# Kernel optimization log

Measured on AMD Instinct MI355X. Metric: run time of the kernel, lower is better.

## Reference

```python
import jax, jax.numpy as jnp
import numpy as np

N_NODES = 20000
N_EDGES = 320000
D_IN = 512
D_OUT = 512


def setup_inputs() -> dict:
    key = jax.random.key(0)
    k1, k2, k3, k4, k5, k6 = jax.random.split(key, 6)
    stdv = 1.0 / np.sqrt(D_OUT)
    return {
        "h": jax.random.normal(k1, (N_NODES, D_IN), dtype=jnp.float32),
        "weight": jax.random.uniform(k2, (D_IN, D_OUT), dtype=jnp.float32, minval=-stdv, maxval=stdv),
        "bias": jax.random.uniform(k3, (D_OUT,), dtype=jnp.float32, minval=-stdv, maxval=stdv),
        # GCN symmetric normalization term per node (deg^{-1/2}); strictly positive
        "norm": jax.random.uniform(k4, (N_NODES, 1), dtype=jnp.float32, minval=0.05, maxval=1.0),
        "src": jax.random.randint(k5, (N_EDGES,), 0, N_NODES, dtype=jnp.int32),
        "dst": jax.random.randint(k6, (N_EDGES,), 0, N_NODES, dtype=jnp.int32),
    }


def reference(h, weight, bias, norm, src, dst):
    # dropout p=0 -> identity (eval mode)
    # pre-normalize after dense projection: [N, d_out]
    hw = norm * jnp.matmul(h, weight)
    # update_all(copy_u, sum): gather source features, scatter-sum into dst
    msg = hw[src]  # [E, d_out]
    agg = jax.ops.segment_sum(msg, dst, num_segments=N_NODES)  # [N, d_out]
    out = agg * norm + bias
    return jax.nn.relu(out)
```

## Files before the change

### kernel.cpp

```cpp
#include <hip/hip_runtime.h>

#define M_NODES 20000
#define N_EDGES_C 320000
#define DIM 512

typedef __attribute__((ext_vector_type(4))) float f32x4;
typedef __attribute__((ext_vector_type(2))) float f32x2;
typedef __attribute__((ext_vector_type(4))) __bf16 bf16x4;
typedef __attribute__((ext_vector_type(8))) __bf16 bf16x8;

__device__ __forceinline__ void async16(__bf16* lds, const __bf16* g) {
  __builtin_amdgcn_global_load_lds(
      (const __attribute__((address_space(1))) void*)g,
      (__attribute__((address_space(3))) void*)lds, 16, 0, 0);
}

__global__ __launch_bounds__(256) void zero_k(int4* __restrict__ counts4) {
  const int i = blockIdx.x * 256 + threadIdx.x;
  if (i < M_NODES / 4) counts4[i] = int4{0, 0, 0, 0};
}

__global__ __launch_bounds__(256) void pre_k(const float* __restrict__ h,
                                             const float* __restrict__ w,
                                             const float* __restrict__ norm,
                                             const int* __restrict__ dst,
                                             __bf16* __restrict__ hb,
                                             __bf16* __restrict__ wT,
                                             int* __restrict__ counts) {
  const int bid = blockIdx.x;
  const int tid = threadIdx.x;
  const int gtid = bid * 256 + tid;
  const int gsz = gridDim.x * 256;

  const int nunits = (M_NODES / 32) * 8;
  for (int u = bid; u < nunits; u += gridDim.x) {
    const int p = u & 7;
    const int row = (u >> 3) * 32 + (tid >> 3);
    const int col = p * 64 + (tid & 7) * 8;
    const float s = norm[row];
    const float* hp = &h[(size_t)row * DIM + col];
    f32x4 v0 = *(const f32x4*)hp;
    f32x4 v1 = *(const f32x4*)(hp + 4);
    bf16x8 o;
    o[0] = (__bf16)(v0.x * s); o[1] = (__bf16)(v0.y * s);
    o[2] = (__bf16)(v0.z * s); o[3] = (__bf16)(v0.w * s);
    o[4] = (__bf16)(v1.x * s); o[5] = (__bf16)(v1.y * s);
    o[6] = (__bf16)(v1.z * s); o[7] = (__bf16)(v1.w * s);
    *(bf16x8*)&hb[(size_t)row * DIM + col] = o;
  }

  if (bid < 256) {
    __shared__ float tile[32][33];
    const int bx = (bid & 15) * 32, by = (bid >> 4) * 32;
    const int tx = tid & 31, ty8 = tid >> 5;
#pragma unroll
    for (int st = 0; st < 4; ++st) {
      const int r = ty8 + st * 8;
      tile[r][tx] = w[(by + r) * DIM + bx + tx];
    }
    __syncthreads();
#pragma unroll
    for (int st = 0; st < 4; ++st) {
      const int r = ty8 + st * 8;
      wT[(bx + r) * DIM + by + tx] = (__bf16)tile[tx][r];
    }
  }

  for (int e = gtid; e < N_EDGES_C; e += gsz) atomicAdd(&counts[dst[e]], 1);
}

__global__ __launch_bounds__(256) void scan_k(int* __restrict__ counts,
                                              int* __restrict__ offsets) {
  __shared__ int wsum2[4];
  const int tid = threadIdx.x;
  const int lane = tid & 63, wid = tid >> 6;
  const int base = tid * 80;
  int s = 0;
  if (tid < 250) {
#pragma unroll
    for (int i = 0; i < 80; i += 4) {
      int4 c = *(const int4*)&counts[base + i];
      s += c.x + c.y + c.z + c.w;
    }
  }
  int x = s;
#pragma unroll
  for (int off = 1; off < 64; off <<= 1) {
    int t = __shfl_up(x, off, 64);
    if (lane >= off) x += t;
  }
  if (lane == 63) wsum2[wid] = x;
  __syncthreads();
  int wbase = 0;
  for (int wI = 0; wI < wid; ++wI) wbase += wsum2[wI];
  int run = wbase + x - s;
  if (tid < 250) {
#pragma unroll
    for (int i = 0; i < 80; i += 4) {
      int4 c = *(const int4*)&counts[base + i];
      int4 o;
      o.x = run;
      o.y = run + c.x;
      o.z = o.y + c.y;
      o.w = o.z + c.z;
      *(int4*)&offsets[base + i] = o;
      *(int4*)&counts[base + i] = o;
      run = o.w + c.w;
    }
  }
  if (tid == 0) {
    int tot = 0;
#pragma unroll
    for (int wI = 0; wI < 4; ++wI) tot += wsum2[wI];
    offsets[M_NODES] = tot;
  }
}

__global__ __launch_bounds__(256) void fill_k(const int* __restrict__ src,
                                              const int* __restrict__ dst,
                                              int* __restrict__ cursor,
                                              int* __restrict__ esrc) {
  int e = blockIdx.x * 256 + threadIdx.x;
  if (e < N_EDGES_C) {
    int p = atomicAdd(&cursor[dst[e]], 1);
    esrc[p] = src[e];
  }
}

__global__ __launch_bounds__(256) void aggregate_k(const __bf16* __restrict__ hb,
                                                   const int* __restrict__ offs,
                                                   const int* __restrict__ esrc,
                                                   __bf16* __restrict__ aggb) {
  const int panel = blockIdx.x & 7;
  const int nb = blockIdx.x >> 3;
  const int wv = threadIdx.x >> 6;
  const int lane = threadIdx.x & 63;
  const int slot = lane >> 3;
  const int cg = lane & 7;
  const int node = nb * 32 + wv * 8 + slot;

  const int beg = offs[node], end = offs[node + 1];
  const size_t pbase = (size_t)panel * 64 + cg * 8;

  f32x2 a2[4] = {};
  int j = beg;
  while (j + 8 <= end) {
    const int idx = esrc[j + cg];
    int sid[8];
#pragma unroll
    for (int g = 0; g < 8; ++g) sid[g] = __shfl(idx, (lane & 56) + g, 64);
#pragma unroll
    for (int g = 0; g < 8; ++g) {
      const uint4 u = *(const uint4*)&hb[(size_t)sid[g] * DIM + pbase];
      f32x2 p0 = {__uint_as_float(u.x << 16), __uint_as_float(u.x & 0xFFFF0000u)};
      f32x2 p1 = {__uint_as_float(u.y << 16), __uint_as_float(u.y & 0xFFFF0000u)};
      f32x2 p2 = {__uint_as_float(u.z << 16), __uint_as_float(u.z & 0xFFFF0000u)};
      f32x2 p3 = {__uint_as_float(u.w << 16), __uint_as_float(u.w & 0xFFFF0000u)};
      a2[0] += p0; a2[1] += p1; a2[2] += p2; a2[3] += p3;
    }
    j += 8;
  }
  for (; j < end; ++j) {
    const uint4 u = *(const uint4*)&hb[(size_t)esrc[j] * DIM + pbase];
    f32x2 p0 = {__uint_as_float(u.x << 16), __uint_as_float(u.x & 0xFFFF0000u)};
    f32x2 p1 = {__uint_as_float(u.y << 16), __uint_as_float(u.y & 0xFFFF0000u)};
    f32x2 p2 = {__uint_as_float(u.z << 16), __uint_as_float(u.z & 0xFFFF0000u)};
    f32x2 p3 = {__uint_as_float(u.w << 16), __uint_as_float(u.w & 0xFFFF0000u)};
    a2[0] += p0; a2[1] += p1; a2[2] += p2; a2[3] += p3;
  }
  bf16x8 o;
#pragma unroll
  for (int q = 0; q < 4; ++q) {
    o[2 * q]     = (__bf16)a2[q].x;
    o[2 * q + 1] = (__bf16)a2[q].y;
  }
  *(bf16x8*)&aggb[(size_t)node * DIM + pbase] = o;
}

__global__ __launch_bounds__(256, 2) void gemm_k(const __bf16* __restrict__ A,
                                                 const __bf16* __restrict__ B,
                                                 const float* __restrict__ bias,
                                                 const float* __restrict__ norm,
                                                 float* __restrict__ C) {
  __shared__ __bf16 As[3][64 * 64];
  __shared__ __bf16 Bs[3][128 * 64];
  const int tid = threadIdx.x;
  const int lane = tid & 63;
  const int wv = tid >> 6;
  const int wr = wv >> 1, wc = wv & 1;
  const int m0 = blockIdx.x * 64;
  const int n0 = blockIdx.y * 128;

  f32x4 acc[2][4] = {};

  const int srow = tid >> 3;
  const int scol = ((tid & 7) ^ (srow & 7)) * 8;
  const int ldst = (tid & 7) * 8;

  auto stage = [&](int buf, int kt) {
    const int kb = kt * 64 + scol;
#pragma unroll
    for (int jj = 0; jj < 2; ++jj) {
      const int lrow = jj * 32 + srow;
      int arow = m0 + lrow;
      arow = arow < M_NODES ? arow : (M_NODES - 1);
      async16(&As[buf][lrow * 64 + ldst], A + (size_t)arow * DIM + kb);
    }
#pragma unroll
    for (int jj = 0; jj < 4; ++jj) {
      const int lrow = jj * 32 + srow;
      async16(&Bs[buf][lrow * 64 + ldst], B + (size_t)(n0 + lrow) * DIM + kb);
    }
  };

  stage(0, 0);
  stage(1, 1);

  int cb = 0;
  for (int kt = 0; kt < DIM / 64; ++kt) {
    if (kt < DIM / 64 - 1)
      asm volatile("s_waitcnt vmcnt(6)" ::: "memory");
    else
      asm volatile("s_waitcnt vmcnt(0)" ::: "memory");
    __builtin_amdgcn_s_barrier();
    asm volatile("" ::: "memory");

    if (kt + 2 < DIM / 64) {
      int sb = cb + 2; if (sb >= 3) sb -= 3;
      stage(sb, kt + 2);
    }

#pragma unroll
    for (int kk = 0; kk < 64; kk += 32) {
      const int c = (kk >> 3) + (lane >> 4);
      bf16x8 af[2], bfr[4];
#pragma unroll
      for (int m = 0; m < 2; ++m) {
        const int r = wr * 32 + m * 16 + (lane & 15);
        af[m] = *(const bf16x8*)&As[cb][r * 64 + ((c ^ (r & 7)) * 8)];
      }
#pragma unroll
      for (int n = 0; n < 4; ++n) {
        const int r = wc * 64 + n * 16 + (lane & 15);
        bfr[n] = *(const bf16x8*)&Bs[cb][r * 64 + ((c ^ (r & 7)) * 8)];
      }
#pragma unroll
      for (int m = 0; m < 2; ++m)
#pragma unroll
        for (int n = 0; n < 4; ++n)
          acc[m][n] = __builtin_amdgcn_mfma_f32_16x16x32_bf16(af[m], bfr[n], acc[m][n], 0, 0, 0);
    }
    cb = (cb == 2) ? 0 : cb + 1;
  }

#pragma unroll
  for (int m = 0; m < 2; ++m) {
    const int rbase = m0 + wr * 32 + m * 16 + (lane >> 4) * 4;
#pragma unroll
    for (int r = 0; r < 4; ++r) {
      const int row = rbase + r;
      if (row < M_NODES) {
        const float nv = norm[row];
#pragma unroll
        for (int n = 0; n < 4; ++n) {
          const int col = n0 + wc * 64 + n * 16 + (lane & 15);
          float v = acc[m][n][r] * nv + bias[col];
          C[(size_t)row * DIM + col] = v > 0.f ? v : 0.f;
        }
      }
    }
  }
}

#define HB_OFF   0UL
#define AGG_OFF  20480000UL
#define WT_OFF   40960000UL
#define CNT_OFF  41484288UL
#define OFS_OFF  41564288UL
#define ESRC_OFF 41644544UL
#define WS_NEEDED 42924544UL

extern "C" void kernel_launch(void* const* d_in, const int* in_sizes, int n_in,
                              void* d_out, int out_size, void* d_ws, size_t ws_size,
                              hipStream_t stream) {
  const float* h    = (const float*)d_in[0];
  const float* w    = (const float*)d_in[1];
  const float* bias = (const float*)d_in[2];
  const float* norm = (const float*)d_in[3];
  const int*   src  = (const int*)d_in[4];
  const int*   dst  = (const int*)d_in[5];
  float* out = (float*)d_out;

  if (ws_size < WS_NEEDED) return;

  char* ws = (char*)d_ws;
  __bf16* hb      = (__bf16*)(ws + HB_OFF);
  __bf16* aggb    = (__bf16*)(ws + AGG_OFF);
  __bf16* wT      = (__bf16*)(ws + WT_OFF);
  int*    counts  = (int*)(ws + CNT_OFF);
  int*    offsets = (int*)(ws + OFS_OFF);
  int*    esrc    = (int*)(ws + ESRC_OFF);

  zero_k<<<20, 256, 0, stream>>>((int4*)counts);
  pre_k<<<2048, 256, 0, stream>>>(h, w, norm, dst, hb, wT, counts);
  scan_k<<<1, 256, 0, stream>>>(counts, offsets);
  fill_k<<<1250, 256, 0, stream>>>(src, dst, counts, esrc);
  aggregate_k<<<5000, 256, 0, stream>>>(hb, offsets, esrc, aggb);
  gemm_k<<<dim3(313, 4), 256, 0, stream>>>(aggb, wT, bias, norm, out);
}
```

Baseline: 120.2 us.

## Restructure final GEMM: full-K A tile in LDS, B streamed from global into registers

The final GEMM becomes 625 blocks, each covering 32 rows and all 512 output columns. Each block loads a whole 32x512 A strip into swizzled LDS once, and each wave streams its 128-column slice of B straight from global memory (L2) into registers, double-buffered across k steps. This removes the triple-buffered LDS pipeline for B, the repeated A loading across four column blocks, and the per-k-tile barriers. In exchange, B fragments are re-read from L2 by every block, register pressure rises (16 accumulators plus 16 B fragments), and the row bounds check is dropped because 20000 divides evenly by 32.

Measured after the change: 144.2 us. +20.0%, slower.

```diff
diff --git a/kernel.cpp b/kernel.cpp
--- a/kernel.cpp
+++ b/kernel.cpp
@@ -177,96 +177,90 @@
   *(bf16x8*)&aggb[(size_t)node * DIM + pbase] = o;
 }
 
-__global__ __launch_bounds__(256, 2) void gemm_k(const __bf16* __restrict__ A,
-                                                 const __bf16* __restrict__ B,
-                                                 const float* __restrict__ bias,
-                                                 const float* __restrict__ norm,
-                                                 float* __restrict__ C) {
-  __shared__ __bf16 As[3][64 * 64];
-  __shared__ __bf16 Bs[3][128 * 64];
+__global__ __launch_bounds__(256) void gemm_k(const __bf16* __restrict__ A,
+                                              const __bf16* __restrict__ B,
+                                              const float* __restrict__ bias,
+                                              const float* __restrict__ norm,
+                                              float* __restrict__ C) {
+  __shared__ __bf16 As[32 * 512];
   const int tid = threadIdx.x;
   const int lane = tid & 63;
   const int wv = tid >> 6;
-  const int wr = wv >> 1, wc = wv & 1;
-  const int m0 = blockIdx.x * 64;
-  const int n0 = blockIdx.y * 128;
-
-  f32x4 acc[2][4] = {};
-
-  const int srow = tid >> 3;
-  const int scol = ((tid & 7) ^ (srow & 7)) * 8;
-  const int ldst = (tid & 7) * 8;
-
-  auto stage = [&](int buf, int kt) {
-    const int kb = kt * 64 + scol;
-#pragma unroll
-    for (int jj = 0; jj < 2; ++jj) {
-      const int lrow = jj * 32 + srow;
-      int arow = m0 + lrow;
-      arow = arow < M_NODES ? arow : (M_NODES - 1);
-      async16(&As[buf][lrow * 64 + ldst], A + (size_t)arow * DIM + kb);
-    }
-#pragma unroll
-    for (int jj = 0; jj < 4; ++jj) {
-      const int lrow = jj * 32 + srow;
-      async16(&Bs[buf][lrow * 64 + ldst], B + (size_t)(n0 + lrow) * DIM + kb);
-    }
-  };
-
-  stage(0, 0);
-  stage(1, 1);
-
-  int cb = 0;
-  for (int kt = 0; kt < DIM / 64; ++kt) {
-    if (kt < DIM / 64 - 1)
-      asm volatile("s_waitcnt vmcnt(6)" ::: "memory");
-    else
-      asm volatile("s_waitcnt vmcnt(0)" ::: "memory");
-    __builtin_amdgcn_s_barrier();
-    asm volatile("" ::: "memory");
-
-    if (kt + 2 < DIM / 64) {
-      int sb = cb + 2; if (sb >= 3) sb -= 3;
-      stage(sb, kt + 2);
-    }
-
-#pragma unroll
-    for (int kk = 0; kk < 64; kk += 32) {
-      const int c = (kk >> 3) + (lane >> 4);
-      bf16x8 af[2], bfr[4];
+  const int m0 = blockIdx.x * 32;
+
+#pragma unroll
+  for (int p = 0; p < 8; ++p) {
+    const int u = p * 256 + tid;
+    const int r = u >> 6;
+    const int c = u & 63;
+    const int g = c ^ (r & 7);
+    async16(&As[r * 512 + c * 8], A + (size_t)(m0 + r) * DIM + g * 8);
+  }
+  __syncthreads();
+
+  f32x4 acc[2][8] = {};
+  const int lr = lane & 15;
+  const int lc = lane >> 4;
+  const __bf16* __restrict__ bbase =
+      B + (size_t)(wv * 128 + lr) * DIM + lc * 8;
+
+  bf16x8 bA[8], bB[8];
+#pragma unroll
+  for (int n = 0; n < 8; ++n)
+    bA[n] = *(const bf16x8*)(bbase + (size_t)n * 16 * DIM);
+
+#pragma unroll
+  for (int kt = 0; kt < 16; kt += 2) {
+#pragma unroll
+    for (int n = 0; n < 8; ++n)
+      bB[n] = *(const bf16x8*)(bbase + (size_t)n * 16 * DIM + (kt + 1) * 32);
+    {
+      const int cr = kt * 4 + lc;
+      bf16x8 af[2];
 #pragma unroll
       for (int m = 0; m < 2; ++m) {
-        const int r = wr * 32 + m * 16 + (lane & 15);
-        af[m] = *(const bf16x8*)&As[cb][r * 64 + ((c ^ (r & 7)) * 8)];
+        const int r = m * 16 + lr;
+        af[m] = *(const bf16x8*)&As[r * 512 + ((cr ^ (r & 7)) * 8)];
       }
 #pragma unroll
-      for (int n = 0; n < 4; ++n) {
-        const int r = wc * 64 + n * 16 + (lane & 15);
-        bfr[n] = *(const bf16x8*)&Bs[cb][r * 64 + ((c ^ (r & 7)) * 8)];
+      for (int m = 0; m < 2; ++m)
+#pragma unroll
+        for (int n = 0; n < 8; ++n)
+          acc[m][n] = __builtin_amdgcn_mfma_f32_16x16x32_bf16(af[m], bA[n], acc[m][n], 0, 0, 0);
+    }
+    if (kt + 2 < 16) {
+#pragma unroll
+      for (int n = 0; n < 8; ++n)
+        bA[n] = *(const bf16x8*)(bbase + (size_t)n * 16 * DIM + (kt + 2) * 32);
+    }
+    {
+      const int cr = (kt + 1) * 4 + lc;
+      bf16x8 af[2];
+#pragma unroll
+      for (int m = 0; m < 2; ++m) {
+        const int r = m * 16 + lr;
+        af[m] = *(const bf16x8*)&As[r * 512 + ((cr ^ (r & 7)) * 8)];
       }
 #pragma unroll
       for (int m = 0; m < 2; ++m)
 #pragma unroll
-        for (int n = 0; n < 4; ++n)
-          acc[m][n] = __builtin_amdgcn_mfma_f32_16x16x32_bf16(af[m], bfr[n], acc[m][n], 0, 0, 0);
-    }
-    cb = (cb == 2) ? 0 : cb + 1;
+        for (int n = 0; n < 8; ++n)
+          acc[m][n] = __builtin_amdgcn_mfma_f32_16x16x32_bf16(af[m], bB[n], acc[m][n], 0, 0, 0);
+    }
   }
 
 #pragma unroll
   for (int m = 0; m < 2; ++m) {
-    const int rbase = m0 + wr * 32 + m * 16 + (lane >> 4) * 4;
+    const int rbase = m0 + m * 16 + (lane >> 4) * 4;
 #pragma unroll
     for (int r = 0; r < 4; ++r) {
       const int row = rbase + r;
-      if (row < M_NODES) {
-        const float nv = norm[row];
-#pragma unroll
-        for (int n = 0; n < 4; ++n) {
-          const int col = n0 + wc * 64 + n * 16 + (lane & 15);
-          float v = acc[m][n][r] * nv + bias[col];
-          C[(size_t)row * DIM + col] = v > 0.f ? v : 0.f;
-        }
+      const float nv = norm[row];
+#pragma unroll
+      for (int n = 0; n < 8; ++n) {
+        const int col = wv * 128 + n * 16 + (lane & 15);
+        float v = acc[m][n][r] * nv + bias[col];
+        C[(size_t)row * DIM + col] = v > 0.f ? v : 0.f;
       }
     }
   }
@@ -306,5 +300,5 @@
   scan_k<<<1, 256, 0, stream>>>(counts, offsets);
   fill_k<<<1250, 256, 0, stream>>>(src, dst, counts, esrc);
   aggregate_k<<<5000, 256, 0, stream>>>(hb, offsets, esrc, aggb);
-  gemm_k<<<dim3(313, 4), 256, 0, stream>>>(aggb, wT, bias, norm, out);
-}
+  gemm_k<<<625, 256, 0, stream>>>(aggb, wT, bias, norm, out);
+}
```
